# Performance work log

Hardware: AMD Instinct MI355X
Metric: run time of the kernel (lower is better)

## Reference

```python
import jax, jax.numpy as jnp
import numpy as np

EMBED_DIM = 512
NUM_HEADS = 8
GLOBAL_MIX = 0.5


def setup_inputs() -> dict:
    key = jax.random.key(0)
    ks = jax.random.split(key, 7)
    B, L, E = 8, 1024, EMBED_DIM
    s = 1.0 / np.sqrt(E)
    x = jax.random.normal(ks[0], (B, L, E), dtype=jnp.float32)
    mask = jax.random.randint(ks[1], (B, L), 0, 2) > 0  # True = valid token
    Wq = jax.random.normal(ks[2], (E, E), dtype=jnp.float32) * s
    Wk = jax.random.normal(ks[3], (E, E), dtype=jnp.float32) * s
    Wv = jax.random.normal(ks[4], (E, E), dtype=jnp.float32) * s
    Wo = jax.random.normal(ks[5], (E, E), dtype=jnp.float32) * s
    G = jax.random.normal(ks[6], (L, L), dtype=jnp.float32)
    return {"x": x, "mask": mask, "Wq": Wq, "Wk": Wk, "Wv": Wv, "Wo": Wo, "G": G}


def _tanh_mha(x, mask, Wq, Wk, Wv, Wo, G):
    B, L, E = x.shape
    H = NUM_HEADS
    D = E // H
    scale = 1.0 / np.sqrt(D)
    dt = x.dtype
    fmax = jnp.finfo(dt).max
    tiny = jnp.finfo(dt).tiny

    def split_heads(t):  # (B,L,E) -> (B,H,L,D)
        return t.reshape(B, L, H, D).transpose(0, 2, 1, 3)

    q = split_heads(x @ Wq.T)
    k = split_heads(x @ Wk.T)
    v = split_heads(x @ Wv.T)

    scores = jnp.tanh(jnp.einsum('bhqd,bhkd->bhqk', q, k) * scale)
    key_valid = mask[:, None, None, :]  # (B,1,1,L)
    scores = jnp.where(key_valid, scores, -jnp.inf)

    finite = jnp.isfinite(scores)
    finite_scores = jnp.where(finite, scores, -fmax)
    m = jnp.max(finite_scores, axis=(1, 2, 3), keepdims=True)  # per-sample amax over heads+q+k
    m = jnp.where(jnp.isfinite(m), m, jnp.zeros_like(m))
    exp_scores = jnp.where(finite, jnp.exp(scores - m), jnp.zeros_like(scores))

    mf = mask.astype(dt)
    exp_scores = exp_scores * mf[:, None, None, :] * mf[:, None, :, None]
    denom = jnp.maximum(exp_scores.sum(axis=(1, 2, 3), keepdims=True), tiny)
    weights = exp_scores / denom
    # dropout p=0 -> identity; renorm pass kept for faithfulness
    renorm = jnp.maximum(weights.sum(axis=(1, 2, 3), keepdims=True), tiny)
    weights = weights / renorm

    # learnable global attention: softmax rows, clamp, mask, normalize over (q,k)
    activated = jnp.maximum(jax.nn.softmax(G, axis=-1), 0.0)  # (L,L)
    gscores = activated[None] * mf[:, None, :] * mf[:, :, None]  # (B,L,L)
    gsums = jnp.maximum(gscores.sum(axis=(1, 2), keepdims=True), tiny)
    gnorm = (gscores / gsums)[:, None]  # (B,1,L,L)
    weights = (1.0 - GLOBAL_MIX) * weights + GLOBAL_MIX * gnorm

    attended = jnp.einsum('bhqk,bhkd->bhqd', weights, v)
    attended = attended * mf[:, None, :, None]
    attended = attended.transpose(0, 2, 1, 3).reshape(B, L, E)
    return attended @ Wo.T


def reference(x, mask, Wq, Wk, Wv, Wo, G):
    return _tanh_mha(x, mask, Wq, Wk, Wv, Wo, G)
```

## Files before the change

kernel.cpp:

```cpp
#include <hip/hip_runtime.h>
#include <math.h>

#define B_ 8
#define L_ 1024
#define E_ 512
#define H_ 8
#define D_ 64
#define QSZ (B_*H_*L_*D_)
#define BLE ((size_t)B_*L_*E_)
#define TINYF 1.175494350822287508e-38f
#define SWK(r) ((((r) ^ ((r) >> 3))) & 7)

typedef unsigned short u16;
typedef __attribute__((ext_vector_type(8))) short bfrag;
typedef __attribute__((ext_vector_type(4))) float ffrag;
typedef __attribute__((ext_vector_type(16))) float ffrag16;
typedef __attribute__((ext_vector_type(4))) short vshort4;

#if __has_builtin(__builtin_amdgcn_exp2f)
#define EXP2F(x) __builtin_amdgcn_exp2f(x)
#else
#define EXP2F(x) __expf((x) * 0.6931471805599453f)
#endif
#if __has_builtin(__builtin_amdgcn_rcpf)
#define RCPF(x) __builtin_amdgcn_rcpf(x)
#else
#define RCPF(x) (1.0f / (x))
#endif

__device__ __forceinline__ u16 f2b(float f) {
  unsigned u = __float_as_uint(f);
  u += 0x7fffu + ((u >> 16) & 1u);
  return (u16)(u >> 16);
}
__device__ __forceinline__ unsigned pk2(float a, float b) {
  unsigned ua = __float_as_uint(a); ua += 0x7fffu + ((ua >> 16) & 1u);
  unsigned ub = __float_as_uint(b); ub += 0x7fffu + ((ub >> 16) & 1u);
  return (ua >> 16) | (ub & 0xffff0000u);
}
__device__ __forceinline__ float blo(unsigned u) { return __uint_as_float(u << 16); }
__device__ __forceinline__ float bhi(unsigned u) { return __uint_as_float(u & 0xffff0000u); }

__device__ __forceinline__ bfrag cvt8v(const float* __restrict__ src) {
  float4 a = *(const float4*)src;
  float4 b = *(const float4*)(src + 4);
  bfrag r;
  r[0]=(short)f2b(a.x); r[1]=(short)f2b(a.y); r[2]=(short)f2b(a.z); r[3]=(short)f2b(a.w);
  r[4]=(short)f2b(b.x); r[5]=(short)f2b(b.y); r[6]=(short)f2b(b.z); r[7]=(short)f2b(b.w);
  return r;
}

__device__ __forceinline__ void gll16(const void* g, void* l) {
  __builtin_amdgcn_global_load_lds(
      (const __attribute__((address_space(1))) void*)g,
      (__attribute__((address_space(3))) void*)l, 16, 0, 0);
}

__global__ __launch_bounds__(256) void prep_softmax_k(
    const float* __restrict__ x, const float* __restrict__ Wq,
    const float* __restrict__ Wk, const float* __restrict__ Wv,
    const float* __restrict__ Wo, const float* __restrict__ G,
    const int* __restrict__ mask,
    u16* __restrict__ xb, u16* __restrict__ Wb, u16* __restrict__ actb,
    float* __restrict__ R, int* __restrict__ posb, int* __restrict__ nvb) {
  const int bid = blockIdx.x, t = threadIdx.x;
  __shared__ float sred[8];
  __shared__ float rred[4][8];
  __shared__ int sc[256];
  if (bid < 2048) {
    size_t c = (size_t)bid * 256 + t;
    *(bfrag*)&xb[c * 8] = cvt8v(x + c * 8);
    return;
  }
  if (bid < 2560) {
    const int c2 = bid - 2048;
    const float* src = (c2 < 128) ? Wq : (c2 < 256) ? Wk : (c2 < 384) ? Wv : Wo;
    const size_t base = (size_t)(c2 >> 7) * 262144;
    const size_t cc = (size_t)(c2 & 127) * 256 + t;
    *(bfrag*)&Wb[base + cc * 8] = cvt8v(src + cc * 8);
    return;
  }
  if (bid >= 3584) {
    const int bb = bid - 3584;
    int4 mi = *(const int4*)(mask + bb * 1024 + t * 4);
    const int vx = mi.x ? 1 : 0, vy = mi.y ? 1 : 0;
    const int vz = mi.z ? 1 : 0, vw = mi.w ? 1 : 0;
    const int c0 = vx + vy + vz + vw;
    sc[t] = c0;
    __syncthreads();
#pragma unroll
    for (int off = 1; off < 256; off <<= 1) {
      int v = (t >= off) ? sc[t - off] : 0;
      __syncthreads();
      sc[t] += v;
      __syncthreads();
    }
    const int nvtot = sc[255];
    int pv = sc[t] - c0;
    int pi = t * 4 - pv;
    int4 pq;
    pq.x = vx ? pv : nvtot + pi; pv += vx; pi += 1 - vx;
    pq.y = vy ? pv : nvtot + pi; pv += vy; pi += 1 - vy;
    pq.z = vz ? pv : nvtot + pi; pv += vz; pi += 1 - vz;
    pq.w = vw ? pv : nvtot + pi;
    *(int4*)(posb + bb * 1024 + t * 4) = pq;
    if (t == 0) nvb[bb] = nvtot;
    return;
  }
  const int q = bid - 2560;
  const int w = t >> 6, lane = t & 63;
  float4 g4 = ((const float4*)(G + (size_t)q * 1024))[t];
  float m = fmaxf(fmaxf(g4.x, g4.y), fmaxf(g4.z, g4.w));
#pragma unroll
  for (int off = 32; off > 0; off >>= 1) m = fmaxf(m, __shfl_down(m, off));
  if (lane == 0) sred[w] = m;
  __syncthreads();
  m = fmaxf(fmaxf(sred[0], sred[1]), fmaxf(sred[2], sred[3]));
  float e0 = __expf(g4.x - m), e1 = __expf(g4.y - m);
  float e2 = __expf(g4.z - m), e3 = __expf(g4.w - m);
  float s = e0 + e1 + e2 + e3;
#pragma unroll
  for (int off = 32; off > 0; off >>= 1) s += __shfl_down(s, off);
  if (lane == 0) sred[4 + w] = s;
  __syncthreads();
  const float inv = 1.0f / (sred[4] + sred[5] + sred[6] + sred[7]);
  const unsigned p0 = pk2(e0 * inv, e1 * inv);
  const unsigned p1 = pk2(e2 * inv, e3 * inv);
  *(uint2*)&actb[(size_t)q * 1024 + t * 4] = make_uint2(p0, p1);
  const float r0 = blo(p0), r1 = bhi(p0);
  const float r2 = blo(p1), r3 = bhi(p1);
  float rd[8];
#pragma unroll
  for (int b = 0; b < 8; ++b) {
    const int* mkp = mask + b * 1024 + t * 4;
    rd[b] = (mkp[0] ? r0 : 0.f) + (mkp[1] ? r1 : 0.f) +
            (mkp[2] ? r2 : 0.f) + (mkp[3] ? r3 : 0.f);
#pragma unroll
    for (int off = 32; off > 0; off >>= 1) rd[b] += __shfl_down(rd[b], off);
  }
  if (lane == 0)
#pragma unroll
    for (int b = 0; b < 8; ++b) rred[w][b] = rd[b];
  __syncthreads();
  if (t < 8) R[q * 8 + t] = rred[0][t] + rred[1][t] + rred[2][t] + rred[3][t];
}

__global__ __launch_bounds__(256) void proj_k(
    const u16* __restrict__ xb, const u16* __restrict__ Wb,
    const int* __restrict__ mask, const float* __restrict__ R,
    const int* __restrict__ posb,
    float* __restrict__ sums,
    u16* __restrict__ Qb, u16* __restrict__ Kb, u16* __restrict__ Vtb) {
  const int m0 = blockIdx.x * 128;
  const int n0 = blockIdx.y * 128;
  __shared__ __align__(16) u16 As[128 * 64];
  __shared__ __align__(16) u16 Bs[128 * 64];
  __shared__ float rr[4][8];
  const int t = threadIdx.x, w = t >> 6, lane = t & 63;
  const int l15 = lane & 15, quad = lane >> 4;
  const int mq = (w >> 1) * 64, nq = (w & 1) * 64;

  if (blockIdx.x == 0 && blockIdx.y == 0) {
    float a8[8] = {0,0,0,0,0,0,0,0};
    for (int q = t; q < 1024; q += 256)
#pragma unroll
      for (int b = 0; b < 8; ++b)
        if (mask[b * 1024 + q]) a8[b] += R[q * 8 + b];
#pragma unroll
    for (int b = 0; b < 8; ++b) {
#pragma unroll
      for (int off = 32; off > 0; off >>= 1) a8[b] += __shfl_down(a8[b], off);
    }
    if (lane == 0)
#pragma unroll
      for (int b = 0; b < 8; ++b) rr[w][b] = a8[b];
    __syncthreads();
    if (t < 8) {
      sums[t] = 0.0f;
      sums[8 + t] = rr[0][t] + rr[1][t] + rr[2][t] + rr[3][t];
    }
  }

  const ffrag fz = {0.f, 0.f, 0.f, 0.f};
  ffrag acc[4][4];
#pragma unroll
  for (int i = 0; i < 4; ++i)
#pragma unroll
    for (int j = 0; j < 4; ++j) acc[i][j] = fz;

  for (int kk = 0; kk < 512; kk += 64) {
    __syncthreads();
#pragma unroll
    for (int j = 0; j < 4; ++j) {
      const int c = w * 256 + j * 64 + lane;
      const int row = c >> 3, ck = (c & 7) ^ (row & 7);
      gll16(xb + (size_t)(m0 + row) * 512 + kk + ck * 8,
            &As[(size_t)(w * 256 + j * 64) * 8]);
    }
#pragma unroll
    for (int j = 0; j < 4; ++j) {
      const int c = w * 256 + j * 64 + lane;
      const int row = c >> 3, ck = (c & 7) ^ (row & 7);
      gll16(Wb + (size_t)(n0 + row) * 512 + kk + ck * 8,
            &Bs[(size_t)(w * 256 + j * 64) * 8]);
    }
    __syncthreads();
#pragma unroll
    for (int s = 0; s < 2; ++s) {
      bfrag av[4], bv[4];
#pragma unroll
      for (int i = 0; i < 4; ++i) {
        const int ar = mq + i * 16 + l15;
        av[i] = *(const bfrag*)&As[ar * 64 + (((quad + 4 * s) ^ (ar & 7)) << 3)];
        const int br = nq + i * 16 + l15;
        bv[i] = *(const bfrag*)&Bs[br * 64 + (((quad + 4 * s) ^ (br & 7)) << 3)];
      }
#pragma unroll
      for (int i = 0; i < 4; ++i)
#pragma unroll
        for (int j = 0; j < 4; ++j)
          acc[i][j] = __builtin_amdgcn_mfma_f32_16x16x32_bf16(av[i], bv[j], acc[i][j], 0, 0, 0);
    }
  }
  const int z = n0 >> 9;
  const int c0 = n0 & 511;
#pragma unroll
  for (int i = 0; i < 4; ++i) {
    const int mbase = m0 + mq + i * 16 + quad * 4;
    const int b = mbase >> 10, l0 = mbase & 1023;
    int4 pr;
    if (z == 0) pr = *(const int4*)(posb + b * 1024 + l0);
#pragma unroll
    for (int j = 0; j < 4; ++j) {
      const int nc = c0 + nq + j * 16 + l15;
      const int h = nc >> 6, d = nc & 63;
      if (z == 0) {
        u16* dst = Qb + (size_t)(b * 8 + h) * 65536 + d;
        dst[(size_t)pr.x * 64] = f2b(acc[i][j][0]);
        dst[(size_t)pr.y * 64] = f2b(acc[i][j][1]);
        dst[(size_t)pr.z * 64] = f2b(acc[i][j][2]);
        dst[(size_t)pr.w * 64] = f2b(acc[i][j][3]);
      } else if (z == 1) {
        u16* dst = Kb + ((size_t)(b * 8 + h) * 1024 + l0) * 64 + d;
#pragma unroll
        for (int r = 0; r < 4; ++r) dst[(size_t)r * 64] = f2b(acc[i][j][r]);
      } else {
        vshort4 vs;
#pragma unroll
        for (int r = 0; r < 4; ++r)
          vs[r] = (short)(mask[b * 1024 + l0 + r] ? f2b(acc[i][j][r]) : (u16)0);
        *(vshort4*)(Vtb + ((size_t)(b * 8 + h) * 64 + d) * 1024 + l0) = vs;
      }
    }
  }
}

__global__ __launch_bounds__(256) void attn_gv_k(
    const u16* __restrict__ Qb, const u16* __restrict__ Kb,
    const u16* __restrict__ Vtb, const u16* __restrict__ actb,
    const int* __restrict__ mask, const int* __restrict__ nvb,
    u16* __restrict__ AEb, u16* __restrict__ AGb, float* __restrict__ denom) {
  __shared__ __align__(16) u16 POOL[13320];
  const int t = threadIdx.x, w = t >> 6, lane = t & 63;
  const int l15 = lane & 15, quad = lane >> 4;

  if (blockIdx.x < 512) {
    u16* As = POOL;
    u16* Bs = POOL + 4096;
    const int mt = blockIdx.x & 127, nt = blockIdx.x >> 7;
    const int m0 = mt * 64, n0 = nt * 128;
    const int b = mt >> 4;
    const int q0 = (mt & 15) * 64;
    const int mq = (w >> 1) * 32, nq = (w & 1) * 64;
    const ffrag fz = {0.f, 0.f, 0.f, 0.f};
    ffrag acc[2][4];
#pragma unroll
    for (int i = 0; i < 2; ++i)
#pragma unroll
      for (int j = 0; j < 4; ++j) acc[i][j] = fz;

    for (int kk = 0; kk < 1024; kk += 64) {
      __syncthreads();
#pragma unroll
      for (int j = 0; j < 2; ++j) {
        const int c = w * 128 + j * 64 + lane;
        const int row = c >> 3, ck = (c & 7) ^ (row & 7);
        gll16(actb + (size_t)(q0 + row) * 1024 + kk + ck * 8,
              &As[(size_t)(w * 128 + j * 64) * 8]);
      }
#pragma unroll
      for (int j = 0; j < 4; ++j) {
        const int c = w * 256 + j * 64 + lane;
        const int row = c >> 3, ck = (c & 7) ^ (row & 7);
        gll16(Vtb + (size_t)(b * 512 + n0 + row) * 1024 + kk + ck * 8,
              &Bs[(size_t)(w * 256 + j * 64) * 8]);
      }
      __syncthreads();
#pragma unroll
      for (int s = 0; s < 2; ++s) {
        bfrag av[2], bv[4];
#pragma unroll
        for (int i = 0; i < 2; ++i) {
          const int ar = mq + i * 16 + l15;
          av[i] = *(const bfrag*)&As[ar * 64 + (((quad + 4 * s) ^ (ar & 7)) << 3)];
        }
#pragma unroll
        for (int j = 0; j < 4; ++j) {
          const int br = nq + j * 16 + l15;
          bv[j] = *(const bfrag*)&Bs[br * 64 + (((quad + 4 * s) ^ (br & 7)) << 3)];
        }
#pragma unroll
        for (int i = 0; i < 2; ++i)
#pragma unroll
          for (int j = 0; j < 4; ++j)
            acc[i][j] = __builtin_amdgcn_mfma_f32_16x16x32_bf16(av[i], bv[j], acc[i][j], 0, 0, 0);
      }
    }
#pragma unroll
    for (int i = 0; i < 2; ++i) {
      const int mbase = m0 + mq + i * 16 + quad * 4;
#pragma unroll
      for (int j = 0; j < 4; ++j) {
        const int n = n0 + nq + j * 16 + l15;
#pragma unroll
        for (int r = 0; r < 4; ++r)
          AGb[(size_t)(mbase + r) * 512 + n] = f2b(acc[i][j][r]);
      }
    }
    return;
  }

  const int aid = blockIdx.x - 512;
  const int qt = aid & 15;
  const int bh = aid >> 4;
  const int b = bh >> 3, h = bh & 7;
  const int nv = nvb[b];
  if (qt * 64 >= nv) return;
  u16* Ks = POOL;
  u16* Vs = POOL + 4096;
  u16* Es = POOL + 8192;
  u16* Ms = POOL + 12288;
  float* red4 = (float*)(POOL + 13312);
  const int l31 = lane & 31, hi = lane >> 5;
  const int qsb = w >> 1, msb = w & 1;
  const int qpb = w & 1, dpb = w >> 1;

  const u16* Kg = Kb + (size_t)bh * 65536;
  const u16* Vg = Vtb + (size_t)bh * 65536;

  const u16* Qrow = Qb + ((size_t)bh * 1024 + qt * 64 + qsb * 32 + l31) * 64;
  bfrag qf[4];
#pragma unroll
  for (int ko = 0; ko < 4; ++ko) qf[ko] = *(const bfrag*)(Qrow + ko * 16 + hi * 8);

  {
    int4 mi = *(const int4*)(mask + b * 1024 + t * 4);
    vshort4 mv;
    mv[0] = mi.x ? (short)0x3F80 : (short)0; mv[1] = mi.y ? (short)0x3F80 : (short)0;
    mv[2] = mi.z ? (short)0x3F80 : (short)0; mv[3] = mi.w ? (short)0x3F80 : (short)0;
    *(vshort4*)&Ms[t * 4] = mv;
  }

  auto stageK = [&](int kt) {
#pragma unroll
    for (int j = 0; j < 2; ++j) {
      const int c = w * 128 + j * 64 + lane;
      const int row = c >> 3, ck = (c & 7) ^ SWK(row);
      gll16(Kg + (size_t)(kt * 64 + row) * 64 + ck * 8,
            &Ks[(size_t)(w * 128 + j * 64) * 8]);
    }
  };
  auto stageV = [&](int kt) {
#pragma unroll
    for (int j = 0; j < 2; ++j) {
      const int c = w * 128 + j * 64 + lane;
      const int row = c >> 3, ck = (c & 7) ^ SWK(row);
      gll16(Vg + (size_t)row * 1024 + kt * 64 + ck * 8,
            &Vs[(size_t)(w * 128 + j * 64) * 8]);
    }
  };

  stageK(0); stageV(0);
  __syncthreads();

  ffrag16 accE, dacc;
#pragma unroll
  for (int i = 0; i < 16; ++i) { accE[i] = 0.f; dacc[i] = 0.f; }

  for (int kt = 0; kt < 16; ++kt) {
    ffrag16 st;
#pragma unroll
    for (int i = 0; i < 16; ++i) st[i] = 0.f;
    const int krow = msb * 32 + l31;
    const int kk7 = SWK(krow);
#pragma unroll
    for (int ko = 0; ko < 4; ++ko) {
      bfrag ak = *(const bfrag*)&Ks[krow * 64 + (((ko * 2 + hi) ^ kk7) << 3)];
      st = __builtin_amdgcn_mfma_f32_32x32x16_bf16(ak, qf[ko], st, 0, 0, 0);
    }
    const int qrow = qsb * 32 + l31;
    const int qk7 = SWK(qrow);
#pragma unroll
    for (int g = 0; g < 4; ++g) {
      float ee[4];
#pragma unroll
      for (int r = 0; r < 4; ++r) {
        const float tt = EXP2F(st[4 * g + r] * 0.360673760222f);
        ee[r] = EXP2F(RCPF(tt + 1.0f) * -2.88539008178f);
      }
      const int k0 = msb * 32 + g * 8 + hi * 4;
      *(uint2*)&Es[qrow * 64 + (((k0 >> 3) ^ qk7) << 3) + (k0 & 7)] =
          make_uint2(pk2(ee[0], ee[1]), pk2(ee[2], ee[3]));
    }
    __syncthreads();
    if (kt < 15) stageK(kt + 1);

    const int erow = qpb * 32 + l31;
    const int ek7 = SWK(erow);
    const int vrow = dpb * 32 + l31;
    const int vk7 = SWK(vrow);
#pragma unroll
    for (int ko = 0; ko < 4; ++ko) {
      const int co = ko * 2 + hi;
      bfrag ea = *(const bfrag*)&Es[erow * 64 + ((co ^ ek7) << 3)];
      bfrag bv = *(const bfrag*)&Vs[vrow * 64 + ((co ^ vk7) << 3)];
      accE = __builtin_amdgcn_mfma_f32_32x32x16_bf16(ea, bv, accE, 0, 0, 0);
      if (dpb == 0) {
        bfrag bm = *(const bfrag*)&Ms[kt * 64 + ko * 16 + hi * 8];
        dacc = __builtin_amdgcn_mfma_f32_32x32x16_bf16(ea, bm, dacc, 0, 0, 0);
      }
    }
    __syncthreads();
    if (kt < 15) stageV(kt + 1);
  }

  const size_t obase = ((size_t)(b * 1024 + qt * 64 + qpb * 32)) * 512
                       + h * 64 + dpb * 32 + l31;
#pragma unroll
  for (int r = 0; r < 16; ++r) {
    const int qloc = (r & 3) + 8 * (r >> 2) + 4 * hi;
    AEb[obase + (size_t)qloc * 512] = f2b(accE[r]);
  }
  float dsumv = 0.0f;
  if (l31 == 0 && dpb == 0) {
    const int cq0 = qt * 64 + qpb * 32 + 4 * hi;
#pragma unroll
    for (int r = 0; r < 16; ++r) {
      const int cq = cq0 + (r & 3) + 8 * (r >> 2);
      dsumv += (cq < nv) ? dacc[r] : 0.0f;
    }
    red4[qpb * 2 + hi] = dsumv;
  }
  __syncthreads();
  if (t == 0) atomicAdd(denom + b, red4[0] + red4[1] + red4[2] + red4[3]);
}

__global__ __launch_bounds__(256) void o_proj_k(
    const u16* __restrict__ AEb, const u16* __restrict__ AGb,
    const int* __restrict__ mask, const int* __restrict__ posb,
    const float* __restrict__ sums,
    const u16* __restrict__ Wb, float* __restrict__ out) {
  const int m0 = blockIdx.x * 128;
  const int n0 = blockIdx.y * 128;
  const int b = m0 >> 10;
  const float c1 = 0.5f / fmaxf(sums[b], TINYF);
  const float c2 = 0.5f / fmaxf(sums[8 + b], TINYF);
  __shared__ __align__(16) u16 As[128 * 64];
  __shared__ __align__(16) u16 Bs[128 * 64];
  const int t = threadIdx.x, w = t >> 6, lane = t & 63;
  const int l15 = lane & 15, quad = lane >> 4;
  const int mq = (w >> 1) * 64, nq = (w & 1) * 64;
  int rowi[4], prw[4], mrow[4]; float c1r[4], c2r[4];
#pragma unroll
  for (int i = 0; i < 4; ++i) {
    const int c = t + i * 256;
    rowi[i] = c >> 3;
    const int tok = (m0 + rowi[i]) & 1023;
    mrow[i] = mask[b * 1024 + tok];
    prw[i] = posb[b * 1024 + tok];
    c1r[i] = mrow[i] ? c1 : 0.0f;
    c2r[i] = mrow[i] ? c2 : 0.0f;
  }
  const ffrag fz = {0.f, 0.f, 0.f, 0.f};
  ffrag acc[4][4];
#pragma unroll
  for (int i = 0; i < 4; ++i)
#pragma unroll
    for (int j = 0; j < 4; ++j) acc[i][j] = fz;

  for (int kk = 0; kk < 512; kk += 64) {
    __syncthreads();
#pragma unroll
    for (int i = 0; i < 4; ++i) {
      const int c = t + i * 256;
      const int row = rowi[i], ck = c & 7;
      const size_t gofs = (size_t)(m0 + row) * 512 + kk + ck * 8;
      const size_t gofsE = (size_t)(b * 1024 + prw[i]) * 512 + kk + ck * 8;
      uint4 ua = *(const uint4*)(AEb + gofsE);
      if (!mrow[i]) ua = make_uint4(0u, 0u, 0u, 0u);
      uint4 ug = *(const uint4*)(AGb + gofs);
      const float a1 = c1r[i], a2 = c2r[i];
      uint4 res;
      res.x = pk2(a1 * blo(ua.x) + a2 * blo(ug.x), a1 * bhi(ua.x) + a2 * bhi(ug.x));
      res.y = pk2(a1 * blo(ua.y) + a2 * blo(ug.y), a1 * bhi(ua.y) + a2 * bhi(ug.y));
      res.z = pk2(a1 * blo(ua.z) + a2 * blo(ug.z), a1 * bhi(ua.z) + a2 * bhi(ug.z));
      res.w = pk2(a1 * blo(ua.w) + a2 * blo(ug.w), a1 * bhi(ua.w) + a2 * bhi(ug.w));
      *(uint4*)&As[row * 64 + ((ck ^ (row & 7)) << 3)] = res;
    }
#pragma unroll
    for (int j = 0; j < 4; ++j) {
      const int c = w * 256 + j * 64 + lane;
      const int row = c >> 3, ck = (c & 7) ^ (row & 7);
      gll16(Wb + (size_t)(1536 + n0 + row) * 512 + kk + ck * 8,
            &Bs[(size_t)(w * 256 + j * 64) * 8]);
    }
    __syncthreads();
#pragma unroll
    for (int s = 0; s < 2; ++s) {
      bfrag av[4], bv[4];
#pragma unroll
      for (int i = 0; i < 4; ++i) {
        const int ar = mq + i * 16 + l15;
        av[i] = *(const bfrag*)&As[ar * 64 + (((quad + 4 * s) ^ (ar & 7)) << 3)];
        const int br = nq + i * 16 + l15;
        bv[i] = *(const bfrag*)&Bs[br * 64 + (((quad + 4 * s) ^ (br & 7)) << 3)];
      }
#pragma unroll
      for (int i = 0; i < 4; ++i)
#pragma unroll
        for (int j = 0; j < 4; ++j)
          acc[i][j] = __builtin_amdgcn_mfma_f32_16x16x32_bf16(av[i], bv[j], acc[i][j], 0, 0, 0);
    }
  }
#pragma unroll
  for (int i = 0; i < 4; ++i) {
    const int mbase = m0 + mq + i * 16 + quad * 4;
#pragma unroll
    for (int j = 0; j < 4; ++j) {
      const int n = n0 + nq + j * 16 + l15;
#pragma unroll
      for (int r = 0; r < 4; ++r)
        out[(size_t)(mbase + r) * 512 + n] = acc[i][j][r];
    }
  }
}

extern "C" void kernel_launch(void* const* d_in, const int* in_sizes, int n_in,
                              void* d_out, int out_size, void* d_ws, size_t ws_size,
                              hipStream_t stream) {
  const float* x  = (const float*)d_in[0];
  const int* mask = (const int*)d_in[1];
  const float* Wq = (const float*)d_in[2];
  const float* Wk = (const float*)d_in[3];
  const float* Wv = (const float*)d_in[4];
  const float* Wo = (const float*)d_in[5];
  const float* G  = (const float*)d_in[6];
  float* out = (float*)d_out;

  u16* xb   = (u16*)d_ws;
  u16* Wb   = xb + (size_t)8192 * 512;
  u16* Qb   = Wb + (size_t)2048 * 512;
  u16* Kb   = Qb + QSZ;
  u16* Vtb  = Kb + QSZ;
  u16* actb = Vtb + QSZ;
  u16* AEb  = actb + (size_t)1024 * 1024;
  u16* AGb  = AEb + BLE;
  float* R  = (float*)(AGb + BLE);
  float* SUMS = R + 8192;
  int* posb = (int*)(SUMS + 16);
  int* nvb  = posb + 8192;

  prep_softmax_k<<<3592, 256, 0, stream>>>(x, Wq, Wk, Wv, Wo, G, mask, xb, Wb, actb, R, posb, nvb);
  proj_k<<<dim3(64, 12), 256, 0, stream>>>(xb, Wb, mask, R, posb, SUMS, Qb, Kb, Vtb);
  attn_gv_k<<<1536, 256, 0, stream>>>(Qb, Kb, Vtb, actb, mask, nvb, AEb, AGb, SUMS);
  o_proj_k<<<dim3(64, 4), 256, 0, stream>>>(AEb, AGb, mask, posb, SUMS, Wb, out);
}
```

Before: 183.7 us.

## Compact keys and values by validity to skip masked key tiles in attention

Keys and values are now written in compacted token order, valid tokens first, using the existing position map, and an inverse token map is built. The attention kernel then loops only over key tiles that contain valid tokens. The mask vector is generated from the valid count instead of being staged in LDS. The global-attention GEMM also skips query tiles past the valid count and gathers rows through the inverse map. This removes the work spent on masked keys and queries, at the cost of scattered writes in the projection epilogue and an extra compacted V buffer.

```diff
diff --git a/kernel.cpp b/kernel.cpp
--- a/kernel.cpp
+++ b/kernel.cpp
@@ -62,7 +62,8 @@
     const float* __restrict__ Wo, const float* __restrict__ G,
     const int* __restrict__ mask,
     u16* __restrict__ xb, u16* __restrict__ Wb, u16* __restrict__ actb,
-    float* __restrict__ R, int* __restrict__ posb, int* __restrict__ nvb) {
+    float* __restrict__ R, int* __restrict__ posb, int* __restrict__ nvb,
+    int* __restrict__ itok) {
   const int bid = blockIdx.x, t = threadIdx.x;
   __shared__ float sred[8];
   __shared__ float rred[4][8];
@@ -104,6 +105,10 @@
     pq.z = vz ? pv : nvtot + pi; pv += vz; pi += 1 - vz;
     pq.w = vw ? pv : nvtot + pi;
     *(int4*)(posb + bb * 1024 + t * 4) = pq;
+    itok[bb * 1024 + pq.x] = t * 4;
+    itok[bb * 1024 + pq.y] = t * 4 + 1;
+    itok[bb * 1024 + pq.z] = t * 4 + 2;
+    itok[bb * 1024 + pq.w] = t * 4 + 3;
     if (t == 0) nvb[bb] = nvtot;
     return;
   }
@@ -150,7 +155,8 @@
     const int* __restrict__ mask, const float* __restrict__ R,
     const int* __restrict__ posb,
     float* __restrict__ sums,
-    u16* __restrict__ Qb, u16* __restrict__ Kb, u16* __restrict__ Vtb) {
+    u16* __restrict__ Qb, u16* __restrict__ Kb, u16* __restrict__ Vtb,
+    u16* __restrict__ Vc) {
   const int m0 = blockIdx.x * 128;
   const int n0 = blockIdx.y * 128;
   __shared__ __align__(16) u16 As[128 * 64];
@@ -228,8 +234,7 @@
   for (int i = 0; i < 4; ++i) {
     const int mbase = m0 + mq + i * 16 + quad * 4;
     const int b = mbase >> 10, l0 = mbase & 1023;
-    int4 pr;
-    if (z == 0) pr = *(const int4*)(posb + b * 1024 + l0);
+    const int4 pr = *(const int4*)(posb + b * 1024 + l0);
 #pragma unroll
     for (int j = 0; j < 4; ++j) {
       const int nc = c0 + nq + j * 16 + l15;
@@ -241,15 +246,20 @@
         dst[(size_t)pr.z * 64] = f2b(acc[i][j][2]);
         dst[(size_t)pr.w * 64] = f2b(acc[i][j][3]);
       } else if (z == 1) {
-        u16* dst = Kb + ((size_t)(b * 8 + h) * 1024 + l0) * 64 + d;
-#pragma unroll
-        for (int r = 0; r < 4; ++r) dst[(size_t)r * 64] = f2b(acc[i][j][r]);
+        u16* dst = Kb + (size_t)(b * 8 + h) * 65536 + d;
+        dst[(size_t)pr.x * 64] = f2b(acc[i][j][0]);
+        dst[(size_t)pr.y * 64] = f2b(acc[i][j][1]);
+        dst[(size_t)pr.z * 64] = f2b(acc[i][j][2]);
+        dst[(size_t)pr.w * 64] = f2b(acc[i][j][3]);
       } else {
         vshort4 vs;
 #pragma unroll
         for (int r = 0; r < 4; ++r)
           vs[r] = (short)(mask[b * 1024 + l0 + r] ? f2b(acc[i][j][r]) : (u16)0);
         *(vshort4*)(Vtb + ((size_t)(b * 8 + h) * 64 + d) * 1024 + l0) = vs;
+        u16* vdst = Vc + ((size_t)(b * 8 + h) * 64 + d) * 1024;
+        vdst[pr.x] = (u16)vs[0]; vdst[pr.y] = (u16)vs[1];
+        vdst[pr.z] = (u16)vs[2]; vdst[pr.w] = (u16)vs[3];
       }
     }
   }
@@ -257,10 +267,11 @@
 
 __global__ __launch_bounds__(256) void attn_gv_k(
     const u16* __restrict__ Qb, const u16* __restrict__ Kb,
-    const u16* __restrict__ Vtb, const u16* __restrict__ actb,
-    const int* __restrict__ mask, const int* __restrict__ nvb,
+    const u16* __restrict__ Vtb, const u16* __restrict__ Vc,
+    const u16* __restrict__ actb,
+    const int* __restrict__ nvb, const int* __restrict__ itok,
     u16* __restrict__ AEb, u16* __restrict__ AGb, float* __restrict__ denom) {
-  __shared__ __align__(16) u16 POOL[13320];
+  __shared__ __align__(16) u16 POOL[12296];
   const int t = threadIdx.x, w = t >> 6, lane = t & 63;
   const int l15 = lane & 15, quad = lane >> 4;
 
@@ -271,6 +282,9 @@
     const int m0 = mt * 64, n0 = nt * 128;
     const int b = mt >> 4;
     const int q0 = (mt & 15) * 64;
+    const int nv = nvb[b];
+    if (q0 >= nv) return;
+    const int* it = itok + b * 1024;
     const int mq = (w >> 1) * 32, nq = (w & 1) * 64;
     const ffrag fz = {0.f, 0.f, 0.f, 0.f};
     ffrag acc[2][4];
@@ -279,13 +293,20 @@
 #pragma unroll
       for (int j = 0; j < 4; ++j) acc[i][j] = fz;
 
+    int tokr[2];
+#pragma unroll
+    for (int j = 0; j < 2; ++j) {
+      const int c = w * 128 + j * 64 + lane;
+      tokr[j] = it[q0 + (c >> 3)];
+    }
+
     for (int kk = 0; kk < 1024; kk += 64) {
       __syncthreads();
 #pragma unroll
       for (int j = 0; j < 2; ++j) {
         const int c = w * 128 + j * 64 + lane;
         const int row = c >> 3, ck = (c & 7) ^ (row & 7);
-        gll16(actb + (size_t)(q0 + row) * 1024 + kk + ck * 8,
+        gll16(actb + (size_t)tokr[j] * 1024 + kk + ck * 8,
               &As[(size_t)(w * 128 + j * 64) * 8]);
       }
 #pragma unroll
@@ -336,30 +357,22 @@
   const int b = bh >> 3, h = bh & 7;
   const int nv = nvb[b];
   if (qt * 64 >= nv) return;
+  const int ktmax = (nv + 63) >> 6;
   u16* Ks = POOL;
   u16* Vs = POOL + 4096;
   u16* Es = POOL + 8192;
-  u16* Ms = POOL + 12288;
-  float* red4 = (float*)(POOL + 13312);
+  float* red4 = (float*)(POOL + 12288);
   const int l31 = lane & 31, hi = lane >> 5;
   const int qsb = w >> 1, msb = w & 1;
   const int qpb = w & 1, dpb = w >> 1;
 
   const u16* Kg = Kb + (size_t)bh * 65536;
-  const u16* Vg = Vtb + (size_t)bh * 65536;
+  const u16* Vg = Vc + (size_t)bh * 65536;
 
   const u16* Qrow = Qb + ((size_t)bh * 1024 + qt * 64 + qsb * 32 + l31) * 64;
   bfrag qf[4];
 #pragma unroll
   for (int ko = 0; ko < 4; ++ko) qf[ko] = *(const bfrag*)(Qrow + ko * 16 + hi * 8);
-
-  {
-    int4 mi = *(const int4*)(mask + b * 1024 + t * 4);
-    vshort4 mv;
-    mv[0] = mi.x ? (short)0x3F80 : (short)0; mv[1] = mi.y ? (short)0x3F80 : (short)0;
-    mv[2] = mi.z ? (short)0x3F80 : (short)0; mv[3] = mi.w ? (short)0x3F80 : (short)0;
-    *(vshort4*)&Ms[t * 4] = mv;
-  }
 
   auto stageK = [&](int kt) {
 #pragma unroll
@@ -387,7 +400,7 @@
 #pragma unroll
   for (int i = 0; i < 16; ++i) { accE[i] = 0.f; dacc[i] = 0.f; }
 
-  for (int kt = 0; kt < 16; ++kt) {
+  for (int kt = 0; kt < ktmax; ++kt) {
     ffrag16 st;
 #pragma unroll
     for (int i = 0; i < 16; ++i) st[i] = 0.f;
@@ -413,7 +426,7 @@
           make_uint2(pk2(ee[0], ee[1]), pk2(ee[2], ee[3]));
     }
     __syncthreads();
-    if (kt < 15) stageK(kt + 1);
+    if (kt < ktmax - 1) stageK(kt + 1);
 
     const int erow = qpb * 32 + l31;
     const int ek7 = SWK(erow);
@@ -426,12 +439,16 @@
       bfrag bv = *(const bfrag*)&Vs[vrow * 64 + ((co ^ vk7) << 3)];
       accE = __builtin_amdgcn_mfma_f32_32x32x16_bf16(ea, bv, accE, 0, 0, 0);
       if (dpb == 0) {
-        bfrag bm = *(const bfrag*)&Ms[kt * 64 + ko * 16 + hi * 8];
+        const int kbase = kt * 64 + ko * 16 + hi * 8;
+        bfrag bm;
+#pragma unroll
+        for (int jj = 0; jj < 8; ++jj)
+          bm[jj] = (short)((kbase + jj < nv) ? 0x3F80 : 0);
         dacc = __builtin_amdgcn_mfma_f32_32x32x16_bf16(ea, bm, dacc, 0, 0, 0);
       }
     }
     __syncthreads();
-    if (kt < 15) stageV(kt + 1);
+    if (kt < ktmax - 1) stageV(kt + 1);
   }
 
   const size_t obase = ((size_t)(b * 1024 + qt * 64 + qpb * 32)) * 512
@@ -494,11 +511,13 @@
     for (int i = 0; i < 4; ++i) {
       const int c = t + i * 256;
       const int row = rowi[i], ck = c & 7;
-      const size_t gofs = (size_t)(m0 + row) * 512 + kk + ck * 8;
       const size_t gofsE = (size_t)(b * 1024 + prw[i]) * 512 + kk + ck * 8;
       uint4 ua = *(const uint4*)(AEb + gofsE);
-      if (!mrow[i]) ua = make_uint4(0u, 0u, 0u, 0u);
-      uint4 ug = *(const uint4*)(AGb + gofs);
+      uint4 ug = *(const uint4*)(AGb + gofsE);
+      if (!mrow[i]) {
+        ua = make_uint4(0u, 0u, 0u, 0u);
+        ug = make_uint4(0u, 0u, 0u, 0u);
+      }
       const float a1 = c1r[i], a2 = c2r[i];
       uint4 res;
       res.x = pk2(a1 * blo(ua.x) + a2 * blo(ug.x), a1 * bhi(ua.x) + a2 * bhi(ug.x));
@@ -569,9 +588,11 @@
   float* SUMS = R + 8192;
   int* posb = (int*)(SUMS + 16);
   int* nvb  = posb + 8192;
-
-  prep_softmax_k<<<3592, 256, 0, stream>>>(x, Wq, Wk, Wv, Wo, G, mask, xb, Wb, actb, R, posb, nvb);
-  proj_k<<<dim3(64, 12), 256, 0, stream>>>(xb, Wb, mask, R, posb, SUMS, Qb, Kb, Vtb);
-  attn_gv_k<<<1536, 256, 0, stream>>>(Qb, Kb, Vtb, actb, mask, nvb, AEb, AGb, SUMS);
+  int* itok = nvb + 8;
+  u16* Vc   = (u16*)(itok + 8192);
+
+  prep_softmax_k<<<3592, 256, 0, stream>>>(x, Wq, Wk, Wv, Wo, G, mask, xb, Wb, actb, R, posb, nvb, itok);
+  proj_k<<<dim3(64, 12), 256, 0, stream>>>(xb, Wb, mask, R, posb, SUMS, Qb, Kb, Vtb, Vc);
+  attn_gv_k<<<1536, 256, 0, stream>>>(Qb, Kb, Vtb, Vc, actb, nvb, itok, AEb, AGb, SUMS);
   o_proj_k<<<dim3(64, 4), 256, 0, stream>>>(AEb, AGb, mask, posb, SUMS, Wb, out);
 }
```

Result: slower. 190.7 us (+3.8%).
